# Kernel optimization log

Measured on AMD Instinct MI355X. Metric: run time of the kernel, lower is better.

The kernel has to match this reference:

```python
import jax, jax.numpy as jnp
import numpy as np

T = 5            # Newton-Schulz iterations
NORM_GROUPS = 16 # groups along out_channels
EPS = 1e-5


def setup_inputs() -> dict:
    key = jax.random.key(0)
    # conv weight: [out_ch, in_ch, kh, kw]
    weight = jax.random.normal(key, (2048, 1024, 3, 3), dtype=jnp.float32) * 0.05
    return {"weight": weight}


def reference(weight):
    g = NORM_GROUPS
    out_ch = weight.shape[0]
    Z = weight.reshape(g, out_ch // g, -1)                 # [g, n, d]
    Zc = Z - Z.mean(axis=-1, keepdims=True)                # center each row
    S = jnp.einsum('gnd,gmd->gnm', Zc, Zc)                 # [g, n, n] covariance
    n = S.shape[-1]
    eye = jnp.eye(n, dtype=S.dtype)
    S = S + EPS * eye
    norm_S = jnp.sqrt(jnp.sum(S * S, axis=(1, 2), keepdims=True))  # fro norm, [g,1,1]
    S = S / norm_S

    B0 = jnp.broadcast_to(eye, S.shape)                    # B[0] = I

    def body(B, _):
        B3 = B @ B @ B                                     # matrix_power3
        Bn = 1.5 * B - 0.5 * (B3 @ S)                      # baddbmm(1.5, B, -0.5, B^3, S)
        return Bn, None

    Bt, _ = jax.lax.scan(body, B0, None, length=T)
    W = (Bt @ Zc) / jnp.sqrt(norm_S)                       # [g, n, d]
    return W.reshape(weight.shape)
```

## Files before the change

### kernel.cpp

```cpp
#include <hip/hip_runtime.h>


#define G 16
#define NROW 128
#define D 9216
#define OC 2048
#define KSPLIT 16
#define KCHUNK 576
#define EPSV 1e-5f

typedef float f32x16 __attribute__((ext_vector_type(16)));
typedef __bf16 bf16x8 __attribute__((ext_vector_type(8)));

union Frag {
    uint4 q;
    unsigned short s[8];
    bf16x8 v;
};

static __device__ __forceinline__ unsigned short f2bf(float x) {
    union { float f; unsigned int u; } a; a.f = x;
    unsigned int u = a.u;
    unsigned int r = u + 0x7FFFu + ((u >> 16) & 1u);
    return (unsigned short)(r >> 16);
}

static __device__ __forceinline__ int swz(int r, int c) {
    return (r << 7) + ((((c >> 3) ^ (r & 15)) << 3) | (c & 7));
}

__global__ __launch_bounds__(256) void k_center(const float* __restrict__ W,
                                                unsigned short* __restrict__ Zc) {
    int row = blockIdx.x;
    int t = threadIdx.x;
    const float4* wp = (const float4*)(W + (size_t)row * D);
    float4 v[9];
    float s = 0.f;
#pragma unroll
    for (int i = 0; i < 9; i++) {
        v[i] = wp[t + i * 256];
        s += v[i].x + v[i].y + v[i].z + v[i].w;
    }
#pragma unroll
    for (int o = 32; o > 0; o >>= 1) s += __shfl_down(s, o, 64);
    __shared__ float ls[4];
    if ((t & 63) == 0) ls[t >> 6] = s;
    __syncthreads();
    float mean = (ls[0] + ls[1] + ls[2] + ls[3]) * (1.0f / 9216.0f);
    ushort4* zp = (ushort4*)(Zc + (size_t)row * D);
#pragma unroll
    for (int i = 0; i < 9; i++) {
        ushort4 o4;
        o4.x = f2bf(v[i].x - mean);
        o4.y = f2bf(v[i].y - mean);
        o4.z = f2bf(v[i].z - mean);
        o4.w = f2bf(v[i].w - mean);
        zp[t + i * 256] = o4;
    }
}

__global__ __launch_bounds__(256) void k_sgemm(const unsigned short* __restrict__ Zc,
                                               float* __restrict__ Spart) {
    __shared__ unsigned short tile[NROW * 128];
    int bid = blockIdx.x;
    int g = bid / KSPLIT, ks = bid % KSPLIT;
    int t = threadIdx.x, lane = t & 63, wave = t >> 6;
    int mq = (wave & 1) * 64, nq = (wave >> 1) * 64;
    int m = lane & 31, h = lane >> 5;

    f32x16 acc[2][2];
#pragma unroll
    for (int i = 0; i < 2; i++)
#pragma unroll
        for (int j = 0; j < 2; j++)
#pragma unroll
            for (int z = 0; z < 16; z++) acc[i][j][z] = 0.f;

    const unsigned short* zg = Zc + (size_t)g * NROW * D + ks * KCHUNK;

    uint4 pf[8];
#pragma unroll
    for (int p = 0; p < 8; p++) {
        int flat = p * 256 + t, r = flat >> 4, gc = flat & 15;
        pf[p] = *(const uint4*)(zg + (size_t)r * D + gc * 8);
    }

    for (int step = 0; step < 5; step++) {
        __syncthreads();
        if (step < 4) {
#pragma unroll
            for (int p = 0; p < 8; p++) {
                int flat = p * 256 + t, r = flat >> 4, gc = flat & 15;
                *(uint4*)(tile + swz(r, gc * 8)) = pf[p];
            }
        } else {
#pragma unroll
            for (int p = 0; p < 4; p++) {
                int flat = p * 256 + t, r = flat >> 3, gc = flat & 7;
                *(uint4*)(tile + swz(r, gc * 8)) = pf[p];
            }
        }
        __syncthreads();
        if (step < 3) {
            int dbase = (step + 1) * 128;
#pragma unroll
            for (int p = 0; p < 8; p++) {
                int flat = p * 256 + t, r = flat >> 4, gc = flat & 15;
                pf[p] = *(const uint4*)(zg + (size_t)r * D + dbase + gc * 8);
            }
        } else if (step == 3) {
#pragma unroll
            for (int p = 0; p < 4; p++) {
                int flat = p * 256 + t, r = flat >> 3, gc = flat & 7;
                pf[p] = *(const uint4*)(zg + (size_t)r * D + 512 + gc * 8);
            }
        }
        int kmax = (step < 4) ? 8 : 4;
#pragma unroll
        for (int kk = 0; kk < 8; kk++) {
            if (kk >= kmax) break;
            int kb = kk * 16 + h * 8;
            Frag a0, a1, b0, b1;
            a0.q = *(const uint4*)(tile + swz(mq + m, kb));
            a1.q = *(const uint4*)(tile + swz(mq + 32 + m, kb));
            b0.q = *(const uint4*)(tile + swz(nq + m, kb));
            b1.q = *(const uint4*)(tile + swz(nq + 32 + m, kb));
            acc[0][0] = __builtin_amdgcn_mfma_f32_32x32x16_bf16(a0.v, b0.v, acc[0][0], 0, 0, 0);
            acc[0][1] = __builtin_amdgcn_mfma_f32_32x32x16_bf16(a0.v, b1.v, acc[0][1], 0, 0, 0);
            acc[1][0] = __builtin_amdgcn_mfma_f32_32x32x16_bf16(a1.v, b0.v, acc[1][0], 0, 0, 0);
            acc[1][1] = __builtin_amdgcn_mfma_f32_32x32x16_bf16(a1.v, b1.v, acc[1][1], 0, 0, 0);
        }
    }
    float* sp = Spart + (size_t)(g * KSPLIT + ks) * 16384;
#pragma unroll
    for (int i = 0; i < 2; i++)
#pragma unroll
        for (int j = 0; j < 2; j++)
#pragma unroll
            for (int reg = 0; reg < 16; reg++) {
                int row = (reg & 3) + 8 * (reg >> 2) + 4 * h;
                sp[(mq + i * 32 + row) * 128 + nq + j * 32 + m] = acc[i][j][reg];
            }
}

__global__ __launch_bounds__(256) void k_reduce(const float* __restrict__ Spart,
                                                float* __restrict__ Sred,
                                                float* __restrict__ normPart) {
    int b = blockIdx.x;
    int g = b >> 4, part = b & 15;
    int el = part * 1024 + threadIdx.x * 4;
    float4 s = {0.f, 0.f, 0.f, 0.f};
    for (int ks = 0; ks < KSPLIT; ks++) {
        float4 p = *(const float4*)(Spart + (size_t)(g * KSPLIT + ks) * 16384 + el);
        s.x += p.x; s.y += p.y; s.z += p.z; s.w += p.w;
    }
    int r = el >> 7, c = el & 127;
    if (r >= c && r <= c + 3) {
        if (r == c) s.x += EPSV;
        else if (r == c + 1) s.y += EPSV;
        else if (r == c + 2) s.z += EPSV;
        else s.w += EPSV;
    }
    *(float4*)(Sred + (size_t)g * 16384 + el) = s;
    float sq = s.x * s.x + s.y * s.y + s.z * s.z + s.w * s.w;
#pragma unroll
    for (int o = 32; o > 0; o >>= 1) sq += __shfl_down(sq, o, 64);
    __shared__ float ls[4];
    if ((threadIdx.x & 63) == 0) ls[threadIdx.x >> 6] = sq;
    __syncthreads();
    if (threadIdx.x == 0) normPart[b] = ls[0] + ls[1] + ls[2] + ls[3];
}

__global__ __launch_bounds__(512) void k_ns(const float* __restrict__ Sred,
                                            const float* __restrict__ normPart,
                                            unsigned short* __restrict__ Bt) {
    extern __shared__ unsigned short sm[];
    unsigned short* Bb = sm;
    unsigned short* Sb = sm + 16384;
    unsigned short* Ub = sm + 32768;
    unsigned short* Vt = sm + 49152;
    int g = blockIdx.x;
    int t = threadIdx.x, lane = t & 63, wave = t >> 6;
    int m = lane & 31, h = lane >> 5;

    float ns = 0.f;
#pragma unroll
    for (int i = 0; i < 16; i++) ns += normPart[g * 16 + i];
    float rn = 1.0f / sqrtf(ns);

    {
        int r = t >> 2, c0 = (t & 3) * 32;
        const float* sp = Sred + (size_t)g * 16384 + r * 128 + c0;
#pragma unroll
        for (int q = 0; q < 4; q++) {
            int c = c0 + q * 8;
            float4 x0 = *(const float4*)(sp + q * 8);
            float4 x1 = *(const float4*)(sp + q * 8 + 4);
            float vv[8] = {x0.x, x0.y, x0.z, x0.w, x1.x, x1.y, x1.z, x1.w};
            Frag fs, fb;
#pragma unroll
            for (int i = 0; i < 8; i++) {
                float sv = vv[i] * rn;
                fs.s[i] = f2bf(sv);
                float bv = -0.5f * sv + ((r == c + i) ? 1.5f : 0.f);
                fb.s[i] = f2bf(bv);
            }
            *(uint4*)(Sb + swz(r, c)) = fs.q;
            *(uint4*)(Bb + swz(r, c)) = fb.q;
        }
    }

    Frag fI[2];
#pragma unroll
    for (int kk2 = 0; kk2 < 2; kk2++)
#pragma unroll
        for (int j = 0; j < 8; j++)
            fI[kk2].s[j] = (m == kk2 * 16 + h * 8 + j) ? (unsigned short)0x3FC0 : (unsigned short)0;

    __syncthreads();

    for (int iter = 0; iter < 4; iter++) {
#pragma unroll
        for (int i = 0; i < 4; i++) {
            int task = wave * 4 + i;
            int tmb = ((task >> 2) & 3) * 32, tnb = (task & 3) * 32;
            const unsigned short* Bsrc = (task < 16) ? Bb : Sb;
            unsigned short* dst = (task < 16) ? Ub : Vt;
            float sc = (task < 16) ? 1.0f : -0.5f;
            f32x16 acc;
#pragma unroll
            for (int z = 0; z < 16; z++) acc[z] = 0.f;
#pragma unroll
            for (int kk = 0; kk < 8; kk++) {
                Frag a, bfr;
                a.q = *(const uint4*)(Bb + swz(tmb + m, kk * 16 + h * 8));
                bfr.q = *(const uint4*)(Bsrc + swz(tnb + m, kk * 16 + h * 8));
                acc = __builtin_amdgcn_mfma_f32_32x32x16_bf16(a.v, bfr.v, acc, 0, 0, 0);
            }
#pragma unroll
            for (int q = 0; q < 4; q++) {
                union { unsigned short s[4]; uint2 u; } pk;
#pragma unroll
                for (int j = 0; j < 4; j++) pk.s[j] = f2bf(sc * acc[q * 4 + j]);
                *(uint2*)(dst + swz(tnb + m, tmb + q * 8 + h * 4)) = pk.u;
            }
        }
        __syncthreads();
        f32x16 acc2[2];
#pragma unroll
        for (int i = 0; i < 2; i++) {
            int task = wave * 2 + i;
            int tmb = (task >> 2) * 32, tnb = (task & 3) * 32;
#pragma unroll
            for (int z = 0; z < 16; z++) acc2[i][z] = 0.f;
#pragma unroll
            for (int kk = 0; kk < 8; kk++) {
                Frag a, bfr;
                a.q = *(const uint4*)(Ub + swz(tmb + m, kk * 16 + h * 8));
                bfr.q = *(const uint4*)(Vt + swz(tnb + m, kk * 16 + h * 8));
                acc2[i] = __builtin_amdgcn_mfma_f32_32x32x16_bf16(a.v, bfr.v, acc2[i], 0, 0, 0);
            }
#pragma unroll
            for (int kk2 = 0; kk2 < 2; kk2++) {
                Frag bfr;
                bfr.q = *(const uint4*)(Bb + swz(tnb + m, tmb + kk2 * 16 + h * 8));
                acc2[i] = __builtin_amdgcn_mfma_f32_32x32x16_bf16(fI[kk2].v, bfr.v, acc2[i], 0, 0, 0);
            }
        }
        __syncthreads();
#pragma unroll
        for (int i = 0; i < 2; i++) {
            int task = wave * 2 + i;
            int tmb = (task >> 2) * 32, tnb = (task & 3) * 32;
#pragma unroll
            for (int q = 0; q < 4; q++) {
                union { unsigned short s[4]; uint2 u; } pk;
#pragma unroll
                for (int j = 0; j < 4; j++) pk.s[j] = f2bf(acc2[i][q * 4 + j]);
                *(uint2*)(Bb + swz(tnb + m, tmb + q * 8 + h * 4)) = pk.u;
            }
        }
        __syncthreads();
    }
    {
        int r = t >> 2, c0 = (t & 3) * 32;
        unsigned short* bp = Bt + (size_t)g * 16384 + r * 128;
#pragma unroll
        for (int q = 0; q < 4; q++) {
            uint4 dd = *(const uint4*)(Bb + swz(r, c0 + q * 8));
            *(uint4*)(bp + c0 + q * 8) = dd;
        }
    }
}

__global__ __launch_bounds__(256) void k_wgemm(const unsigned short* __restrict__ Zc,
                                               const unsigned short* __restrict__ Bt,
                                               const float* __restrict__ normPart,
                                               float* __restrict__ out) {
    __shared__ unsigned short Ab[16384];
    __shared__ unsigned short Zt[16384];
    int nt = blockIdx.x, g = blockIdx.y;
    int t = threadIdx.x, lane = t & 63, wave = t >> 6;
    int m = lane & 31, h = lane >> 5;

    const unsigned short* bg = Bt + (size_t)g * 16384;
    const unsigned short* zg = Zc + (size_t)g * NROW * D + nt * 128;
#pragma unroll
    for (int p = 0; p < 8; p++) {
        int flat = p * 256 + t;
        int r = flat >> 4, gc = flat & 15;
        uint4 da = *(const uint4*)(bg + r * 128 + gc * 8);
        uint4 dz = *(const uint4*)(zg + (size_t)r * D + gc * 8);
        *(uint4*)(Ab + swz(r, gc * 8)) = da;
        *(uint4*)(Zt + swz(r, gc * 8)) = dz;
    }
    __syncthreads();
    float nsum = 0.f;
#pragma unroll
    for (int i = 0; i < 16; i++) nsum += normPart[g * 16 + i];
    float ss = 1.0f / sqrtf(sqrtf(nsum));

    int cw = wave * 32 + m;

    f32x16 acc[4];
#pragma unroll
    for (int i = 0; i < 4; i++)
#pragma unroll
        for (int z = 0; z < 16; z++) acc[i][z] = 0.f;

#pragma unroll
    for (int ks = 0; ks < 8; ks++) {
        int k0 = ks * 16 + h * 8;
        Frag b;
#pragma unroll
        for (int j = 0; j < 8; j++) b.s[j] = Zt[swz(k0 + j, cw)];
#pragma unroll
        for (int i = 0; i < 4; i++) {
            Frag a;
            a.q = *(const uint4*)(Ab + swz(i * 32 + m, k0));
            acc[i] = __builtin_amdgcn_mfma_f32_32x32x16_bf16(a.v, b.v, acc[i], 0, 0, 0);
        }
    }
    float* og = out + (size_t)(g * NROW) * D + nt * 128 + cw;
#pragma unroll
    for (int i = 0; i < 4; i++)
#pragma unroll
        for (int reg = 0; reg < 16; reg++) {
            int row = i * 32 + (reg & 3) + 8 * (reg >> 2) + 4 * h;
            og[(size_t)row * D] = acc[i][reg] * ss;
        }
}

extern "C" void kernel_launch(void* const* d_in, const int* in_sizes, int n_in,
                              void* d_out, int out_size, void* d_ws, size_t ws_size,
                              hipStream_t stream) {
    const float* W = (const float*)d_in[0];
    float* out = (float*)d_out;
    char* ws = (char*)d_ws;

    unsigned short* Zc = (unsigned short*)(ws);
    float* Spart = (float*)(ws + 37748736ULL);
    float* Sred = (float*)(ws + 54525952ULL);
    float* normPart = (float*)(ws + 55574528ULL);
    unsigned short* Bt = (unsigned short*)(ws + 55575552ULL);

    k_center<<<OC, 256, 0, stream>>>(W, Zc);
    k_sgemm<<<G * KSPLIT, 256, 0, stream>>>(Zc, Spart);
    k_reduce<<<256, 256, 0, stream>>>(Spart, Sred, normPart);
    hipFuncSetAttribute((const void*)k_ns,
                        hipFuncAttributeMaxDynamicSharedMemorySize, 131072);
    k_ns<<<G, 512, 131072, stream>>>(Sred, normPart, Bt);
    k_wgemm<<<dim3(72, G), 256, 0, stream>>>(Zc, Bt, normPart, out);
}
```

Measured before the change: 190.3 us.

## Fold mean-centering into GEMMs via rank-one corrections, drop centering kernel

Removes the separate centering pass. The covariance GEMM now reads raw fp32 weights, converts them to bf16 on the fly, writes raw bf16 Z and accumulates per-row sums. Centering is applied algebraically: S is corrected by subtracting n·mu·muᵀ in the reduce kernel, and the output is corrected by subtracting B·mu in the final GEMM. This saves one full read and write pass over the weights and one launch. The risk is precision: computing Zc·Zcᵀ as Z·Zᵀ minus the mean term with bf16 raw values can cancel poorly when the means are large, and the fp32 loads raise register pressure in the sgemm.

```diff
diff --git a/kernel.cpp b/kernel.cpp
--- a/kernel.cpp
+++ b/kernel.cpp
@@ -25,49 +25,29 @@
     return (unsigned short)(r >> 16);
 }
 
+static __device__ __forceinline__ float bf2f(unsigned short s) {
+    union { unsigned int u; float f; } a; a.u = ((unsigned int)s) << 16;
+    return a.f;
+}
+
 static __device__ __forceinline__ int swz(int r, int c) {
     return (r << 7) + ((((c >> 3) ^ (r & 15)) << 3) | (c & 7));
 }
 
-__global__ __launch_bounds__(256) void k_center(const float* __restrict__ W,
-                                                unsigned short* __restrict__ Zc) {
-    int row = blockIdx.x;
-    int t = threadIdx.x;
-    const float4* wp = (const float4*)(W + (size_t)row * D);
-    float4 v[9];
-    float s = 0.f;
-#pragma unroll
-    for (int i = 0; i < 9; i++) {
-        v[i] = wp[t + i * 256];
-        s += v[i].x + v[i].y + v[i].z + v[i].w;
-    }
-#pragma unroll
-    for (int o = 32; o > 0; o >>= 1) s += __shfl_down(s, o, 64);
-    __shared__ float ls[4];
-    if ((t & 63) == 0) ls[t >> 6] = s;
-    __syncthreads();
-    float mean = (ls[0] + ls[1] + ls[2] + ls[3]) * (1.0f / 9216.0f);
-    ushort4* zp = (ushort4*)(Zc + (size_t)row * D);
-#pragma unroll
-    for (int i = 0; i < 9; i++) {
-        ushort4 o4;
-        o4.x = f2bf(v[i].x - mean);
-        o4.y = f2bf(v[i].y - mean);
-        o4.z = f2bf(v[i].z - mean);
-        o4.w = f2bf(v[i].w - mean);
-        zp[t + i * 256] = o4;
-    }
-}
-
-__global__ __launch_bounds__(256) void k_sgemm(const unsigned short* __restrict__ Zc,
-                                               float* __restrict__ Spart) {
+__global__ __launch_bounds__(256) void k_sgemm(const float* __restrict__ W,
+                                               unsigned short* __restrict__ Zraw,
+                                               float* __restrict__ Spart,
+                                               float* __restrict__ rowsumPart) {
     __shared__ unsigned short tile[NROW * 128];
+    __shared__ float rsum[NROW];
     int bid = blockIdx.x;
-    int g = bid / KSPLIT, ks = bid % KSPLIT;
+    int g = bid >> 4, ks = bid & 15;
     int t = threadIdx.x, lane = t & 63, wave = t >> 6;
     int mq = (wave & 1) * 64, nq = (wave >> 1) * 64;
     int m = lane & 31, h = lane >> 5;
 
+    if (t < 128) rsum[t] = 0.f;
+
     f32x16 acc[2][2];
 #pragma unroll
     for (int i = 0; i < 2; i++)
@@ -76,43 +56,65 @@
 #pragma unroll
             for (int z = 0; z < 16; z++) acc[i][j][z] = 0.f;
 
-    const unsigned short* zg = Zc + (size_t)g * NROW * D + ks * KCHUNK;
-
-    uint4 pf[8];
-#pragma unroll
-    for (int p = 0; p < 8; p++) {
-        int flat = p * 256 + t, r = flat >> 4, gc = flat & 15;
-        pf[p] = *(const uint4*)(zg + (size_t)r * D + gc * 8);
+    float rs[16], rsh[8];
+#pragma unroll
+    for (int i = 0; i < 16; i++) rs[i] = 0.f;
+#pragma unroll
+    for (int i = 0; i < 8; i++) rsh[i] = 0.f;
+
+    const float* wg = W + (size_t)g * NROW * D + ks * KCHUNK;
+    unsigned short* zo = Zraw + (size_t)g * NROW * D + ks * KCHUNK;
+
+    float4 pf[16];
+#pragma unroll
+    for (int p = 0; p < 16; p++) {
+        int fl = p * 256 + t, r = fl >> 5, cf = fl & 31;
+        pf[p] = *(const float4*)(wg + (size_t)r * D + cf * 4);
     }
 
     for (int step = 0; step < 5; step++) {
         __syncthreads();
         if (step < 4) {
+            int dbase = step * 128;
+#pragma unroll
+            for (int p = 0; p < 16; p++) {
+                int fl = p * 256 + t, r = fl >> 5, cf = fl & 31;
+                float4 x = pf[p];
+                rs[p] += x.x + x.y + x.z + x.w;
+                ushort4 pk;
+                pk.x = f2bf(x.x); pk.y = f2bf(x.y);
+                pk.z = f2bf(x.z); pk.w = f2bf(x.w);
+                *(ushort4*)(zo + (size_t)r * D + dbase + cf * 4) = pk;
+                union { ushort4 s4; uint2 u; } cv; cv.s4 = pk;
+                *(uint2*)(tile + swz(r, cf * 4)) = cv.u;
+            }
+        } else {
 #pragma unroll
             for (int p = 0; p < 8; p++) {
-                int flat = p * 256 + t, r = flat >> 4, gc = flat & 15;
-                *(uint4*)(tile + swz(r, gc * 8)) = pf[p];
-            }
-        } else {
-#pragma unroll
-            for (int p = 0; p < 4; p++) {
-                int flat = p * 256 + t, r = flat >> 3, gc = flat & 7;
-                *(uint4*)(tile + swz(r, gc * 8)) = pf[p];
+                int fl = p * 256 + t, r = fl >> 4, cf = fl & 15;
+                float4 x = pf[p];
+                rsh[p] += x.x + x.y + x.z + x.w;
+                ushort4 pk;
+                pk.x = f2bf(x.x); pk.y = f2bf(x.y);
+                pk.z = f2bf(x.z); pk.w = f2bf(x.w);
+                *(ushort4*)(zo + (size_t)r * D + 512 + cf * 4) = pk;
+                union { ushort4 s4; uint2 u; } cv; cv.s4 = pk;
+                *(uint2*)(tile + swz(r, cf * 4)) = cv.u;
             }
         }
         __syncthreads();
         if (step < 3) {
             int dbase = (step + 1) * 128;
 #pragma unroll
+            for (int p = 0; p < 16; p++) {
+                int fl = p * 256 + t, r = fl >> 5, cf = fl & 31;
+                pf[p] = *(const float4*)(wg + (size_t)r * D + dbase + cf * 4);
+            }
+        } else if (step == 3) {
+#pragma unroll
             for (int p = 0; p < 8; p++) {
-                int flat = p * 256 + t, r = flat >> 4, gc = flat & 15;
-                pf[p] = *(const uint4*)(zg + (size_t)r * D + dbase + gc * 8);
-            }
-        } else if (step == 3) {
-#pragma unroll
-            for (int p = 0; p < 4; p++) {
-                int flat = p * 256 + t, r = flat >> 3, gc = flat & 7;
-                pf[p] = *(const uint4*)(zg + (size_t)r * D + 512 + gc * 8);
+                int fl = p * 256 + t, r = fl >> 4, cf = fl & 15;
+                pf[p] = *(const float4*)(wg + (size_t)r * D + 512 + cf * 4);
             }
         }
         int kmax = (step < 4) ? 8 : 4;
@@ -131,7 +133,7 @@
             acc[1][1] = __builtin_amdgcn_mfma_f32_32x32x16_bf16(a1.v, b1.v, acc[1][1], 0, 0, 0);
         }
     }
-    float* sp = Spart + (size_t)(g * KSPLIT + ks) * 16384;
+    float* sp = Spart + (size_t)bid * 16384;
 #pragma unroll
     for (int i = 0; i < 2; i++)
 #pragma unroll
@@ -141,20 +143,39 @@
                 int row = (reg & 3) + 8 * (reg >> 2) + 4 * h;
                 sp[(mq + i * 32 + row) * 128 + nq + j * 32 + m] = acc[i][j][reg];
             }
+#pragma unroll
+    for (int p = 0; p < 16; p++) atomicAdd(&rsum[p * 8 + (t >> 5)], rs[p]);
+#pragma unroll
+    for (int p = 0; p < 8; p++) atomicAdd(&rsum[p * 16 + (t >> 4)], rsh[p]);
+    __syncthreads();
+    if (t < 128) rowsumPart[bid * 128 + t] = rsum[t];
 }
 
 __global__ __launch_bounds__(256) void k_reduce(const float* __restrict__ Spart,
+                                                const float* __restrict__ rowsumPart,
                                                 float* __restrict__ Sred,
                                                 float* __restrict__ normPart) {
+    __shared__ float muv[128];
+    __shared__ float ls[4];
     int b = blockIdx.x;
     int g = b >> 4, part = b & 15;
-    int el = part * 1024 + threadIdx.x * 4;
+    int t = threadIdx.x;
+    if (t < 128) {
+        float s = 0.f;
+        for (int ks = 0; ks < KSPLIT; ks++) s += rowsumPart[(g * 16 + ks) * 128 + t];
+        muv[t] = s * (1.0f / 9216.0f);
+    }
+    __syncthreads();
+    int el = part * 1024 + t * 4;
     float4 s = {0.f, 0.f, 0.f, 0.f};
     for (int ks = 0; ks < KSPLIT; ks++) {
         float4 p = *(const float4*)(Spart + (size_t)(g * KSPLIT + ks) * 16384 + el);
         s.x += p.x; s.y += p.y; s.z += p.z; s.w += p.w;
     }
     int r = el >> 7, c = el & 127;
+    float4 mc = *(float4*)&muv[c];
+    float dm = 9216.0f * muv[r];
+    s.x -= dm * mc.x; s.y -= dm * mc.y; s.z -= dm * mc.z; s.w -= dm * mc.w;
     if (r >= c && r <= c + 3) {
         if (r == c) s.x += EPSV;
         else if (r == c + 1) s.y += EPSV;
@@ -165,15 +186,16 @@
     float sq = s.x * s.x + s.y * s.y + s.z * s.z + s.w * s.w;
 #pragma unroll
     for (int o = 32; o > 0; o >>= 1) sq += __shfl_down(sq, o, 64);
-    __shared__ float ls[4];
-    if ((threadIdx.x & 63) == 0) ls[threadIdx.x >> 6] = sq;
-    __syncthreads();
-    if (threadIdx.x == 0) normPart[b] = ls[0] + ls[1] + ls[2] + ls[3];
+    if ((t & 63) == 0) ls[t >> 6] = sq;
+    __syncthreads();
+    if (t == 0) normPart[b] = ls[0] + ls[1] + ls[2] + ls[3];
 }
 
 __global__ __launch_bounds__(512) void k_ns(const float* __restrict__ Sred,
                                             const float* __restrict__ normPart,
-                                            unsigned short* __restrict__ Bt) {
+                                            const float* __restrict__ rowsumPart,
+                                            unsigned short* __restrict__ Bt,
+                                            float* __restrict__ cvec) {
     extern __shared__ unsigned short sm[];
     unsigned short* Bb = sm;
     unsigned short* Sb = sm + 16384;
@@ -209,14 +231,13 @@
             *(uint4*)(Bb + swz(r, c)) = fb.q;
         }
     }
-
     Frag fI[2];
 #pragma unroll
     for (int kk2 = 0; kk2 < 2; kk2++)
 #pragma unroll
         for (int j = 0; j < 8; j++)
-            fI[kk2].s[j] = (m == kk2 * 16 + h * 8 + j) ? (unsigned short)0x3FC0 : (unsigned short)0;
-
+            fI[kk2].s[j] = (m == kk2 * 16 + h * 8 + j) ? (unsigned short)0x3FC0
+                                                       : (unsigned short)0;
     __syncthreads();
 
     for (int iter = 0; iter < 4; iter++) {
@@ -291,20 +312,39 @@
             *(uint4*)(bp + c0 + q * 8) = dd;
         }
     }
-}
-
-__global__ __launch_bounds__(256) void k_wgemm(const unsigned short* __restrict__ Zc,
+    float* muv = (float*)(sm + 32768);
+    if (t < 128) {
+        float s = 0.f;
+        for (int ks = 0; ks < KSPLIT; ks++) s += rowsumPart[(g * 16 + ks) * 128 + t];
+        muv[t] = s * (1.0f / 9216.0f);
+    }
+    __syncthreads();
+    if (t < 128) {
+        float cacc = 0.f;
+        for (int k = 0; k < 128; k++) cacc += bf2f(Bb[swz(t, k)]) * muv[k];
+        cvec[g * 128 + t] = cacc;
+    }
+}
+
+__global__ __launch_bounds__(256) void k_wgemm(const unsigned short* __restrict__ Zraw,
                                                const unsigned short* __restrict__ Bt,
                                                const float* __restrict__ normPart,
+                                               const float* __restrict__ cvec,
                                                float* __restrict__ out) {
     __shared__ unsigned short Ab[16384];
     __shared__ unsigned short Zt[16384];
+    __shared__ float cs[128];
     int nt = blockIdx.x, g = blockIdx.y;
     int t = threadIdx.x, lane = t & 63, wave = t >> 6;
     int m = lane & 31, h = lane >> 5;
 
+    float nsum = 0.f;
+#pragma unroll
+    for (int i = 0; i < 16; i++) nsum += normPart[g * 16 + i];
+    float ss = 1.0f / sqrtf(sqrtf(nsum));
+
     const unsigned short* bg = Bt + (size_t)g * 16384;
-    const unsigned short* zg = Zc + (size_t)g * NROW * D + nt * 128;
+    const unsigned short* zg = Zraw + (size_t)g * NROW * D + nt * 128;
 #pragma unroll
     for (int p = 0; p < 8; p++) {
         int flat = p * 256 + t;
@@ -314,11 +354,8 @@
         *(uint4*)(Ab + swz(r, gc * 8)) = da;
         *(uint4*)(Zt + swz(r, gc * 8)) = dz;
     }
-    __syncthreads();
-    float nsum = 0.f;
-#pragma unroll
-    for (int i = 0; i < 16; i++) nsum += normPart[g * 16 + i];
-    float ss = 1.0f / sqrtf(sqrtf(nsum));
+    if (t < 128) cs[t] = cvec[g * 128 + t] * ss;
+    __syncthreads();
 
     int cw = wave * 32 + m;
 
@@ -347,7 +384,7 @@
 #pragma unroll
         for (int reg = 0; reg < 16; reg++) {
             int row = i * 32 + (reg & 3) + 8 * (reg >> 2) + 4 * h;
-            og[(size_t)row * D] = acc[i][reg] * ss;
+            og[(size_t)row * D] = acc[i][reg] * ss - cs[row];
         }
 }
 
@@ -358,17 +395,18 @@
     float* out = (float*)d_out;
     char* ws = (char*)d_ws;
 
-    unsigned short* Zc = (unsigned short*)(ws);
+    unsigned short* Zraw = (unsigned short*)(ws);
     float* Spart = (float*)(ws + 37748736ULL);
     float* Sred = (float*)(ws + 54525952ULL);
     float* normPart = (float*)(ws + 55574528ULL);
     unsigned short* Bt = (unsigned short*)(ws + 55575552ULL);
-
-    k_center<<<OC, 256, 0, stream>>>(W, Zc);
-    k_sgemm<<<G * KSPLIT, 256, 0, stream>>>(Zc, Spart);
-    k_reduce<<<256, 256, 0, stream>>>(Spart, Sred, normPart);
+    float* rowsumPart = (float*)(ws + 56099840ULL);
+    float* cvec = (float*)(ws + 56230912ULL);
+
+    k_sgemm<<<G * KSPLIT, 256, 0, stream>>>(W, Zraw, Spart, rowsumPart);
+    k_reduce<<<256, 256, 0, stream>>>(Spart, rowsumPart, Sred, normPart);
     hipFuncSetAttribute((const void*)k_ns,
                         hipFuncAttributeMaxDynamicSharedMemorySize, 131072);
-    k_ns<<<G, 512, 131072, stream>>>(Sred, normPart, Bt);
-    k_wgemm<<<dim3(72, G), 256, 0, stream>>>(Zc, Bt, normPart, out);
-}
+    k_ns<<<G, 512, 131072, stream>>>(Sred, normPart, rowsumPart, Bt, cvec);
+    k_wgemm<<<dim3(72, G), 256, 0, stream>>>(Zraw, Bt, normPart, cvec, out);
+}
```

Result: faster. 185.8 us (-2.4%).
